# Kernel optimization log

Measured on AMD Instinct MI355X. Metric: run time of the kernel, lower is better.

Reference implementation:

```python
import jax, jax.numpy as jnp
import numpy as np

N_NODES = 50000
IN_FEAT = 64
HIDDEN = 128
SCALAR_DIM = 64
VECTOR_DIM = 32
N_EDGES = 800000
INPUT_DIM = 3 * IN_FEAT + 1  # 193


def _mlp(x, W1, b1, W2, b2):
    # Linear -> ReLU -> Linear (make_mlp)
    h = jax.nn.relu(x @ W1 + b1)
    return h @ W2 + b2


def setup_inputs() -> dict:
    key = jax.random.key(0)
    ks = jax.random.split(key, 12)
    s = lambda fan_in: 1.0 / np.sqrt(fan_in)
    return {
        "endpoints": jax.random.randint(ks[0], (N_EDGES, 2), 0, N_NODES, dtype=jnp.int64),
        "edge_lengths": jax.random.uniform(ks[1], (N_EDGES, 1), dtype=jnp.float32),
        "midpoint_theta": jax.random.normal(ks[2], (N_EDGES,), dtype=jnp.float32),
        "endpoint_features": jax.random.normal(ks[3], (N_NODES, IN_FEAT), dtype=jnp.float32),
        "W1s": jax.random.normal(ks[4], (INPUT_DIM, HIDDEN), dtype=jnp.float32) * s(INPUT_DIM),
        "b1s": jnp.zeros((HIDDEN,), dtype=jnp.float32),
        "W2s": jax.random.normal(ks[5], (HIDDEN, SCALAR_DIM), dtype=jnp.float32) * s(HIDDEN),
        "b2s": jnp.zeros((SCALAR_DIM,), dtype=jnp.float32),
        "W1v": jax.random.normal(ks[6], (INPUT_DIM, HIDDEN), dtype=jnp.float32) * s(INPUT_DIM),
        "b1v": jnp.zeros((HIDDEN,), dtype=jnp.float32),
        "W2v": jax.random.normal(ks[7], (HIDDEN, VECTOR_DIM), dtype=jnp.float32) * s(HIDDEN),
        "b2v": jnp.zeros((VECTOR_DIM,), dtype=jnp.float32),
    }


def reference(endpoints, edge_lengths, midpoint_theta, endpoint_features,
              W1s, b1s, W2s, b2s, W1v, b1v, W2v, b2v):
    i = endpoints[:, 0]
    j = endpoints[:, 1]
    feat_i = endpoint_features[i]            # [E, F] gather
    feat_j = endpoint_features[j]            # [E, F] gather
    diff = jnp.abs(feat_i - feat_j)          # [E, F]
    inputs = jnp.concatenate([feat_i, feat_j, diff, edge_lengths], axis=-1)  # [E, 3F+1]
    h0 = _mlp(inputs, W1s, b1s, W2s, b2s)    # [E, scalar_dim]
    direction = jnp.stack([jnp.cos(midpoint_theta), jnp.sin(midpoint_theta)], axis=-1)  # [E, 2]
    amplitude = _mlp(inputs, W1v, b1v, W2v, b2v)[..., None]  # [E, vector_dim, 1]
    v0 = amplitude * direction[:, None, :]   # [E, vector_dim, 2]
    return (h0, v0)
```

## Files before the change

### kernel.cpp

```cpp
#include <hip/hip_runtime.h>
#include <hip/hip_bf16.h>

#define N_EDGES 800000
#define M_BLK   64
#define NBLK    (N_EDGES / M_BLK)

typedef __attribute__((ext_vector_type(8))) _Float16 half8;
typedef __attribute__((ext_vector_type(4))) float    f32x4;

__global__ void prep_kernel(const float* __restrict__ W1s, const float* __restrict__ W1v,
                            const float* __restrict__ W2s, const float* __restrict__ W2v,
                            _Float16* __restrict__ wt1s, _Float16* __restrict__ wt1v,
                            _Float16* __restrict__ wt2s, _Float16* __restrict__ wt2v,
                            float* __restrict__ w1s192, float* __restrict__ w1v192)
{
    int idx = blockIdx.x * blockDim.x + threadIdx.x;
    if (idx < 128 * 192) {
        int c = idx / 192, k = idx % 192;
        wt1s[idx] = (_Float16)W1s[k * 128 + c];
        wt1v[idx] = (_Float16)W1v[k * 128 + c];
        return;
    }
    int i2 = idx - 128 * 192;
    if (i2 >= 0 && i2 < 64 * 128) {
        int c = i2 / 128, k = i2 % 128;
        wt2s[i2] = (_Float16)W2s[k * 64 + c];
        return;
    }
    int i3 = idx - (128 * 192 + 64 * 128);
    if (i3 >= 0 && i3 < 32 * 128) {
        int c = i3 / 128, k = i3 % 128;
        wt2v[i3] = (_Float16)W2v[k * 32 + c];
        return;
    }
    int i4 = idx - (128 * 192 + 64 * 128 + 32 * 128);
    if (i4 >= 0 && i4 < 128) {
        w1s192[i4] = W1s[192 * 128 + i4];
        w1v192[i4] = W1v[192 * 128 + i4];
    }
}

__device__ __forceinline__ void* xsw(char* base, int row, int byte_in_row, int row_bytes)
{
    int chunk = byte_in_row >> 4;
    int sw    = ((chunk ^ (row & 7)) << 4) | (byte_in_row & 15);
    return (void*)(base + row * row_bytes + sw);
}

__global__ void edge_mlp_kernel(
    const int*   __restrict__ endpoints,
    const float* __restrict__ edge_len,
    const float* __restrict__ theta,
    const float* __restrict__ feat,
    const float* __restrict__ b1s, const float* __restrict__ b2s,
    const float* __restrict__ b1v, const float* __restrict__ b2v,
    const _Float16* __restrict__ wt1s, const _Float16* __restrict__ wt1v,
    const _Float16* __restrict__ wt2s, const _Float16* __restrict__ wt2v,
    const float* __restrict__ w1s192, const float* __restrict__ w1v192,
    float* __restrict__ h0, float* __restrict__ v0)
{
    __shared__ char   lds[32768];
    __shared__ float  Len[M_BLK];
    __shared__ float2 Dir[M_BLK];
    char* ldsX  = lds;
    char* ldsHs = lds;
    char* ldsHv = lds + 16384;

    const int t   = threadIdx.x;
    const int blk = blockIdx.x;
    const int w   = t >> 6;
    const int l   = t & 63;
    const int lr  = l & 15;
    const int lk  = l >> 4;
    const int e   = t >> 3;
    const int f0q = t & 7;
    const int base = blk * M_BLK;

    const int c1 = w * 16 + lr;

    {
        int2 ep0 = ((const int2*)endpoints)[base + e];
        const float* pfi = feat + (size_t)ep0.x * 64 + f0q * 8;
        const float* pfj = feat + (size_t)ep0.y * 64 + f0q * 8;
        float4 fi0 = ((const float4*)pfi)[0], fi1 = ((const float4*)pfi)[1];
        float4 fj0 = ((const float4*)pfj)[0], fj1 = ((const float4*)pfj)[1];
        float ai[8] = {fi0.x, fi0.y, fi0.z, fi0.w, fi1.x, fi1.y, fi1.z, fi1.w};
        float bj[8] = {fj0.x, fj0.y, fj0.z, fj0.w, fj1.x, fj1.y, fj1.z, fj1.w};
        half8 pi, pj, pd;
#pragma unroll
        for (int q = 0; q < 8; ++q) {
            pi[q] = (_Float16)ai[q];
            pj[q] = (_Float16)bj[q];
            pd[q] = (_Float16)fabsf(ai[q] - bj[q]);
        }
        *(half8*)xsw(ldsX, e, f0q * 16, 384)       = pi;
        *(half8*)xsw(ldsX, e, 128 + f0q * 16, 384) = pj;
        *(half8*)xsw(ldsX, e, 256 + f0q * 16, 384) = pd;
        if (t < M_BLK)          Len[t] = edge_len[base + t];
        else if (t < 2 * M_BLK) {
            float th = theta[base + (t - M_BLK)];
            Dir[t - M_BLK] = make_float2(cosf(th), sinf(th));
        }
    }

    const float b1s_c   = b1s[c1];
    const float b1v_c   = b1v[c1];
    const float w192s_c = w1s192[c1];
    const float w192v_c = w1v192[c1];
    const int rt2 = w >> 1;
    const int ch  = w & 1;
    const float b2s_a = b2s[ch * 32 + lr];
    const float b2s_b = b2s[ch * 32 + 16 + lr];
    const float b2v_c = b2v[ch * 16 + lr];

    __syncthreads();

    f32x4 accs[4], accv[4];
    {
        const char* pws = (const char*)wt1s + c1 * 384 + lk * 16;
        const char* pwv = (const char*)wt1v + c1 * 384 + lk * 16;
#pragma unroll
        for (int rt = 0; rt < 4; ++rt) {
            accs[rt] = (f32x4){0.f, 0.f, 0.f, 0.f};
            accv[rt] = (f32x4){0.f, 0.f, 0.f, 0.f};
        }
        half8 bs = *reinterpret_cast<const half8*>(pws);
        half8 bv = *reinterpret_cast<const half8*>(pwv);
#pragma unroll
        for (int ks = 0; ks < 6; ++ks) {
            half8 bsn = bs, bvn = bv;
            if (ks < 5) {
                bsn = *reinterpret_cast<const half8*>(pws + (ks + 1) * 64);
                bvn = *reinterpret_cast<const half8*>(pwv + (ks + 1) * 64);
            }
#pragma unroll
            for (int rt = 0; rt < 4; ++rt) {
                half8 a = *(half8*)xsw(ldsX, rt * 16 + lr, ks * 64 + lk * 16, 384);
                accs[rt] = __builtin_amdgcn_mfma_f32_16x16x32_f16(a, bs, accs[rt], 0, 0, 0);
                accv[rt] = __builtin_amdgcn_mfma_f32_16x16x32_f16(a, bv, accv[rt], 0, 0, 0);
            }
            bs = bsn; bv = bvn;
        }
    }
    __syncthreads();

#pragma unroll
    for (int rt = 0; rt < 4; ++rt) {
        float4 l4 = *reinterpret_cast<const float4*>(&Len[rt * 16 + lk * 4]);
        float lv[4] = {l4.x, l4.y, l4.z, l4.w};
#pragma unroll
        for (int r = 0; r < 4; ++r) {
            int row = rt * 16 + lk * 4 + r;
            float hs = accs[rt][r] + b1s_c + lv[r] * w192s_c;
            float hv = accv[rt][r] + b1v_c + lv[r] * w192v_c;
            *(_Float16*)xsw(ldsHs, row, c1 * 2, 256) = (_Float16)fmaxf(hs, 0.f);
            *(_Float16*)xsw(ldsHv, row, c1 * 2, 256) = (_Float16)fmaxf(hv, 0.f);
        }
    }
    __syncthreads();

    {
        f32x4 acc2[2];
        acc2[0] = (f32x4){0.f, 0.f, 0.f, 0.f};
        acc2[1] = (f32x4){0.f, 0.f, 0.f, 0.f};
        f32x4 accV = (f32x4){0.f, 0.f, 0.f, 0.f};
        const int cv = ch * 16 + lr;
#pragma unroll
        for (int ks = 0; ks < 4; ++ks) {
            half8 a2 = *(half8*)xsw(ldsHs, rt2 * 16 + lr, ks * 64 + lk * 16, 256);
#pragma unroll
            for (int ct = 0; ct < 2; ++ct) {
                int c2 = ch * 32 + ct * 16 + lr;
                half8 b = *reinterpret_cast<const half8*>(wt2s + c2 * 128 + ks * 32 + lk * 8);
                acc2[ct] = __builtin_amdgcn_mfma_f32_16x16x32_f16(a2, b, acc2[ct], 0, 0, 0);
            }
            half8 av  = *(half8*)xsw(ldsHv, rt2 * 16 + lr, ks * 64 + lk * 16, 256);
            half8 bv2 = *reinterpret_cast<const half8*>(wt2v + cv * 128 + ks * 32 + lk * 8);
            accV = __builtin_amdgcn_mfma_f32_16x16x32_f16(av, bv2, accV, 0, 0, 0);
        }
#pragma unroll
        for (int ct = 0; ct < 2; ++ct) {
            int c2 = ch * 32 + ct * 16 + lr;
            float bias = ct ? b2s_b : b2s_a;
#pragma unroll
            for (int r = 0; r < 4; ++r) {
                int row = rt2 * 16 + lk * 4 + r;
                h0[(size_t)(base + row) * 64 + c2] = acc2[ct][r] + bias;
            }
        }
#pragma unroll
        for (int r = 0; r < 4; ++r) {
            int row = rt2 * 16 + lk * 4 + r;
            float amp = accV[r] + b2v_c;
            float2 d = Dir[row];
            *reinterpret_cast<float2*>(v0 + ((size_t)(base + row) * 32 + cv) * 2) =
                make_float2(amp * d.x, amp * d.y);
        }
    }
}

extern "C" void kernel_launch(void* const* d_in, const int* in_sizes, int n_in,
                              void* d_out, int out_size, void* d_ws, size_t ws_size,
                              hipStream_t stream)
{
    const int*   endpoints = (const int*)d_in[0];
    const float* edge_len  = (const float*)d_in[1];
    const float* theta     = (const float*)d_in[2];
    const float* feat      = (const float*)d_in[3];
    const float* W1s       = (const float*)d_in[4];
    const float* b1s       = (const float*)d_in[5];
    const float* W2s       = (const float*)d_in[6];
    const float* b2s       = (const float*)d_in[7];
    const float* W1v       = (const float*)d_in[8];
    const float* b1v       = (const float*)d_in[9];
    const float* W2v       = (const float*)d_in[10];
    const float* b2v       = (const float*)d_in[11];

    char* ws = (char*)d_ws;
    _Float16* wt1s   = (_Float16*)(ws);
    _Float16* wt1v   = (_Float16*)(ws + 49152);
    _Float16* wt2s   = (_Float16*)(ws + 98304);
    _Float16* wt2v   = (_Float16*)(ws + 114688);
    float*    w1s192 = (float*)(ws + 122880);
    float*    w1v192 = (float*)(ws + 123392);

    prep_kernel<<<145, 256, 0, stream>>>(W1s, W1v, W2s, W2v,
                                         wt1s, wt1v, wt2s, wt2v, w1s192, w1v192);

    float* h0 = (float*)d_out;
    float* v0 = h0 + (size_t)N_EDGES * 64;
    edge_mlp_kernel<<<NBLK, 512, 0, stream>>>(endpoints, edge_len, theta, feat,
                                              b1s, b2s, b1v, b2v,
                                              wt1s, wt1v, wt2s, wt2v,
                                              w1s192, w1v192, h0, v0);
}
```

Baseline: 348.7 us.

## Add per-wave edge MLP kernel with fp16 feature table and register-held inputs

Adds a prep pass that converts node features to fp16 in workspace. A new kernel gives each wave 16 edges and keeps the gathered inputs in registers as MFMA A operands instead of staging them through LDS. Each wave computes all 128 hidden columns and both output MLPs using per-wave LDS only, so no block-wide syncs are needed. This halves gather bandwidth and removes block synchronization. In exchange, every wave rereads both full layer-1 weight matrices from global/L2, and the feature diff is now computed in fp16.

Result: slower. 780.6 us (+123.9%).

```diff
diff --git a/kernel.cpp b/kernel.cpp
--- a/kernel.cpp
+++ b/kernel.cpp
@@ -1,12 +1,17 @@
 #include <hip/hip_runtime.h>
 #include <hip/hip_bf16.h>
 
-#define N_EDGES 800000
-#define M_BLK   64
-#define NBLK    (N_EDGES / M_BLK)
+#define N_EDGES  800000
+#define N_NODES  50000
+#define WAVES_PB 4
+#define EDGES_PW 16
+#define NBLK     (N_EDGES / (WAVES_PB * EDGES_PW))
 
 typedef __attribute__((ext_vector_type(8))) _Float16 half8;
 typedef __attribute__((ext_vector_type(4))) float    f32x4;
+
+#define WS_FEAT16_OFF 131072
+#define WS_NEEDED     (WS_FEAT16_OFF + (size_t)N_NODES * 64 * 2)
 
 __global__ void prep_kernel(const float* __restrict__ W1s, const float* __restrict__ W1v,
                             const float* __restrict__ W2s, const float* __restrict__ W2v,
@@ -40,6 +45,154 @@
     }
 }
 
+__global__ void prep_feat16(const float* __restrict__ feat, _Float16* __restrict__ feat16)
+{
+    int idx = blockIdx.x * blockDim.x + threadIdx.x;
+    if (idx < N_NODES * 32) {
+        float2 v = ((const float2*)feat)[idx];
+        feat16[idx * 2]     = (_Float16)v.x;
+        feat16[idx * 2 + 1] = (_Float16)v.y;
+    }
+}
+
+__device__ __forceinline__ void* xsw16(char* base, int row, int byte_in_row)
+{
+    int sw = ((((byte_in_row >> 4) ^ row) & 15) << 4) | (byte_in_row & 15);
+    return (void*)(base + row * 256 + sw);
+}
+
+__global__ void edge_mlp_wave(
+    const int*   __restrict__ endpoints,
+    const float* __restrict__ edge_len,
+    const float* __restrict__ theta,
+    const _Float16* __restrict__ feat16,
+    const float* __restrict__ b1s, const float* __restrict__ b2s,
+    const float* __restrict__ b1v, const float* __restrict__ b2v,
+    const _Float16* __restrict__ wt1s, const _Float16* __restrict__ wt1v,
+    const _Float16* __restrict__ wt2s, const _Float16* __restrict__ wt2v,
+    const float* __restrict__ w1s192, const float* __restrict__ w1v192,
+    float* __restrict__ h0, float* __restrict__ v0)
+{
+    __shared__ char lds[WAVES_PB * 8192];
+    const int t   = threadIdx.x;
+    const int wid = t >> 6;
+    const int l   = t & 63;
+    const int e16 = l & 15;
+    const int kg  = l >> 4;
+    char* Hs = lds + wid * 8192;
+    char* Hv = Hs + 4096;
+    const int ebase = (blockIdx.x * WAVES_PB + wid) * EDGES_PW;
+
+    int2 ep = ((const int2*)endpoints)[ebase + e16];
+    const _Float16* fi = feat16 + (size_t)ep.x * 64 + kg * 8;
+    const _Float16* fj = feat16 + (size_t)ep.y * 64 + kg * 8;
+    half8 pi0 = *(const half8*)(fi);
+    half8 pi1 = *(const half8*)(fi + 32);
+    half8 pj0 = *(const half8*)(fj);
+    half8 pj1 = *(const half8*)(fj + 32);
+    float4 len4 = *(const float4*)(edge_len + ebase + kg * 4);
+    float4 th4  = *(const float4*)(theta    + ebase + kg * 4);
+
+    half8 pd0, pd1;
+#pragma unroll
+    for (int q = 0; q < 8; ++q) {
+        _Float16 d0 = pi0[q] - pj0[q];
+        _Float16 d1 = pi1[q] - pj1[q];
+        pd0[q] = d0 < (_Float16)0 ? (_Float16)(-d0) : d0;
+        pd1[q] = d1 < (_Float16)0 ? (_Float16)(-d1) : d1;
+    }
+
+    f32x4 accS[8], accV[8];
+#pragma unroll
+    for (int ct = 0; ct < 8; ++ct) {
+        accS[ct] = (f32x4){0.f, 0.f, 0.f, 0.f};
+        accV[ct] = (f32x4){0.f, 0.f, 0.f, 0.f};
+    }
+    const char* bws = (const char*)wt1s + e16 * 384 + kg * 16;
+    const char* bwv = (const char*)wt1v + e16 * 384 + kg * 16;
+#pragma unroll
+    for (int ks = 0; ks < 6; ++ks) {
+        half8 a = (ks == 0) ? pi0 : (ks == 1) ? pi1 : (ks == 2) ? pj0
+                : (ks == 3) ? pj1 : (ks == 4) ? pd0 : pd1;
+#pragma unroll
+        for (int ct = 0; ct < 8; ++ct) {
+            half8 bs = *(const half8*)(bws + ct * 6144 + ks * 64);
+            half8 bv = *(const half8*)(bwv + ct * 6144 + ks * 64);
+            accS[ct] = __builtin_amdgcn_mfma_f32_16x16x32_f16(a, bs, accS[ct], 0, 0, 0);
+            accV[ct] = __builtin_amdgcn_mfma_f32_16x16x32_f16(a, bv, accV[ct], 0, 0, 0);
+        }
+    }
+
+    float lenv[4] = {len4.x, len4.y, len4.z, len4.w};
+#pragma unroll
+    for (int ct = 0; ct < 8; ++ct) {
+        int col = ct * 16 + e16;
+        float bs_ = b1s[col], bv_ = b1v[col];
+        float ws_ = w1s192[col], wv_ = w1v192[col];
+#pragma unroll
+        for (int r = 0; r < 4; ++r) {
+            int row = kg * 4 + r;
+            float hs = accS[ct][r] + bs_ + lenv[r] * ws_;
+            float hv = accV[ct][r] + bv_ + lenv[r] * wv_;
+            *(_Float16*)xsw16(Hs, row, col * 2) = (_Float16)fmaxf(hs, 0.f);
+            *(_Float16*)xsw16(Hv, row, col * 2) = (_Float16)fmaxf(hv, 0.f);
+        }
+    }
+
+    half8 a2s[4], a2v[4];
+#pragma unroll
+    for (int ks = 0; ks < 4; ++ks) {
+        a2s[ks] = *(half8*)xsw16(Hs, e16, ks * 64 + kg * 16);
+        a2v[ks] = *(half8*)xsw16(Hv, e16, ks * 64 + kg * 16);
+    }
+
+    f32x4 o2[4];
+#pragma unroll
+    for (int c2t = 0; c2t < 4; ++c2t) o2[c2t] = (f32x4){0.f, 0.f, 0.f, 0.f};
+    const char* b2s_base = (const char*)wt2s + e16 * 256 + kg * 16;
+#pragma unroll
+    for (int ks = 0; ks < 4; ++ks)
+#pragma unroll
+        for (int c2t = 0; c2t < 4; ++c2t) {
+            half8 b = *(const half8*)(b2s_base + c2t * 4096 + ks * 64);
+            o2[c2t] = __builtin_amdgcn_mfma_f32_16x16x32_f16(a2s[ks], b, o2[c2t], 0, 0, 0);
+        }
+    f32x4 ov[2];
+    ov[0] = (f32x4){0.f, 0.f, 0.f, 0.f};
+    ov[1] = (f32x4){0.f, 0.f, 0.f, 0.f};
+    const char* b2v_base = (const char*)wt2v + e16 * 256 + kg * 16;
+#pragma unroll
+    for (int ks = 0; ks < 4; ++ks)
+#pragma unroll
+        for (int cvt = 0; cvt < 2; ++cvt) {
+            half8 b = *(const half8*)(b2v_base + cvt * 4096 + ks * 64);
+            ov[cvt] = __builtin_amdgcn_mfma_f32_16x16x32_f16(a2v[ks], b, ov[cvt], 0, 0, 0);
+        }
+
+    float thv[4] = {th4.x, th4.y, th4.z, th4.w};
+    float dx[4], dy[4];
+#pragma unroll
+    for (int r = 0; r < 4; ++r) { dx[r] = cosf(thv[r]); dy[r] = sinf(thv[r]); }
+#pragma unroll
+    for (int c2t = 0; c2t < 4; ++c2t) {
+        float bias = b2s[c2t * 16 + e16];
+#pragma unroll
+        for (int r = 0; r < 4; ++r)
+            h0[(size_t)(ebase + kg * 4 + r) * 64 + c2t * 16 + e16] = o2[c2t][r] + bias;
+    }
+#pragma unroll
+    for (int cvt = 0; cvt < 2; ++cvt) {
+        float bias = b2v[cvt * 16 + e16];
+#pragma unroll
+        for (int r = 0; r < 4; ++r) {
+            float amp = ov[cvt][r] + bias;
+            *reinterpret_cast<float2*>(
+                v0 + ((size_t)(ebase + kg * 4 + r) * 32 + cvt * 16 + e16) * 2) =
+                make_float2(amp * dx[r], amp * dy[r]);
+        }
+    }
+}
+
 __device__ __forceinline__ void* xsw(char* base, int row, int byte_in_row, int row_bytes)
 {
     int chunk = byte_in_row >> 4;
@@ -47,7 +200,7 @@
     return (void*)(base + row * row_bytes + sw);
 }
 
-__global__ void edge_mlp_kernel(
+__global__ void edge_mlp_kernel_f32(
     const int*   __restrict__ endpoints,
     const float* __restrict__ edge_len,
     const float* __restrict__ theta,
@@ -60,8 +213,8 @@
     float* __restrict__ h0, float* __restrict__ v0)
 {
     __shared__ char   lds[32768];
-    __shared__ float  Len[M_BLK];
-    __shared__ float2 Dir[M_BLK];
+    __shared__ float  Len[64];
+    __shared__ float2 Dir[64];
     char* ldsX  = lds;
     char* ldsHs = lds;
     char* ldsHv = lds + 16384;
@@ -74,8 +227,7 @@
     const int lk  = l >> 4;
     const int e   = t >> 3;
     const int f0q = t & 7;
-    const int base = blk * M_BLK;
-
+    const int base = blk * 64;
     const int c1 = w * 16 + lr;
 
     {
@@ -96,10 +248,10 @@
         *(half8*)xsw(ldsX, e, f0q * 16, 384)       = pi;
         *(half8*)xsw(ldsX, e, 128 + f0q * 16, 384) = pj;
         *(half8*)xsw(ldsX, e, 256 + f0q * 16, 384) = pd;
-        if (t < M_BLK)          Len[t] = edge_len[base + t];
-        else if (t < 2 * M_BLK) {
-            float th = theta[base + (t - M_BLK)];
-            Dir[t - M_BLK] = make_float2(cosf(th), sinf(th));
+        if (t < 64)           Len[t] = edge_len[base + t];
+        else if (t < 128) {
+            float th = theta[base + (t - 64)];
+            Dir[t - 64] = make_float2(cosf(th), sinf(th));
         }
     }
 
@@ -223,14 +375,26 @@
     _Float16* wt2v   = (_Float16*)(ws + 114688);
     float*    w1s192 = (float*)(ws + 122880);
     float*    w1v192 = (float*)(ws + 123392);
+    _Float16* feat16 = (_Float16*)(ws + WS_FEAT16_OFF);
 
     prep_kernel<<<145, 256, 0, stream>>>(W1s, W1v, W2s, W2v,
                                          wt1s, wt1v, wt2s, wt2v, w1s192, w1v192);
 
     float* h0 = (float*)d_out;
     float* v0 = h0 + (size_t)N_EDGES * 64;
-    edge_mlp_kernel<<<NBLK, 512, 0, stream>>>(endpoints, edge_len, theta, feat,
-                                              b1s, b2s, b1v, b2v,
-                                              wt1s, wt1v, wt2s, wt2v,
-                                              w1s192, w1v192, h0, v0);
-}
+
+    if (ws_size >= WS_NEEDED) {
+        prep_feat16<<<(N_NODES * 32 + 255) / 256, 256, 0, stream>>>(feat, feat16);
+        edge_mlp_wave<<<NBLK, WAVES_PB * 64, 0, stream>>>(
+            endpoints, edge_len, theta, feat16,
+            b1s, b2s, b1v, b2v,
+            wt1s, wt1v, wt2s, wt2v,
+            w1s192, w1v192, h0, v0);
+    } else {
+        edge_mlp_kernel_f32<<<N_EDGES / 64, 512, 0, stream>>>(
+            endpoints, edge_len, theta, feat,
+            b1s, b2s, b1v, b2v,
+            wt1s, wt1v, wt2s, wt2v,
+            w1s192, w1v192, h0, v0);
+    }
+}
```
